# Kernel tuning notes

Hardware: AMD Instinct MI355X
Metric: run time of the kernel (lower is better)

The kernel has to match this reference:

```python
import jax, jax.numpy as jnp
import numpy as np

EPS = 1e-6  # rms_norm_eps
Q_EPS = 1e-5


def activation_quant(x):
    # per-token (last dim) absmax int8 quant
    scale = 127.0 / jnp.clip(jnp.max(jnp.abs(x), axis=-1, keepdims=True), Q_EPS, None)
    return jnp.clip(jnp.round(x * scale), -128, 127) / scale


def weight_quant(w):
    # ternary quant with global mean-absmax scale
    scale = 1.0 / jnp.clip(jnp.mean(jnp.abs(w)), Q_EPS, None)
    return jnp.clip(jnp.round(w * scale), -1, 1) / scale


def bit_linear(x, w):
    # straight-through estimator on both activation and weight quantization
    xq = x + jax.lax.stop_gradient(activation_quant(x) - x)
    wq = w + jax.lax.stop_gradient(weight_quant(w) - w)
    return jnp.einsum('...k,nk->...n', xq, wq)


def rmsnorm(x, w):
    var = jnp.mean(jnp.square(x), axis=-1, keepdims=True)
    return x * jax.lax.rsqrt(var + EPS) * w


def setup_inputs() -> dict:
    key = jax.random.key(0)
    ks = jax.random.split(key, 6)
    B, C, H, D, F, NC = 8, 3, 128, 2048, 8192, 1000
    return {
        'x': jax.random.normal(ks[0], (B, C, H, D), jnp.float32),
        'Wg': jax.random.normal(ks[1], (F, D), jnp.float32) * (D ** -0.5),
        'Wu': jax.random.normal(ks[2], (F, D), jnp.float32) * (D ** -0.5),
        'Wd': jax.random.normal(ks[3], (D, F), jnp.float32) * (F ** -0.5),
        'ln_w': jnp.ones((F,), jnp.float32),
        'cls_W': jax.random.normal(ks[4], (NC, C), jnp.float32) * (C ** -0.5),
        'cls_b': jnp.zeros((NC,), jnp.float32),
    }


def reference(x, Wg, Wu, Wd, ln_w, cls_W, cls_b):
    # BitNet SwiGLU MLP
    h = jax.nn.silu(bit_linear(x, Wg)) * bit_linear(x, Wu)  # [B,3,H,F]
    h = rmsnorm(h, ln_w)
    h = bit_linear(h, Wd)  # [B,3,H,D]
    # classifier: AdaptiveAvgPool2d((1,1)) over last two dims -> [B,3] -> Linear
    pooled = jnp.mean(h, axis=(2, 3))  # [B,3]
    return pooled @ cls_W.T + cls_b  # [B, num_classes]
```

## Files before the change

### kernel.cpp

```cpp
#include <hip/hip_runtime.h>
#include <stdint.h>

#define BB 8
#define CC 3
#define HH 128
#define DD 2048
#define FF 8192
#define NCLS 1000
#define MTOK (BB*CC*HH)
#define NW   (FF*DD)
#define INV_NW (1.0f/16777216.0f)

typedef __attribute__((ext_vector_type(4))) int i32x4;
typedef _Float16 f16x8 __attribute__((ext_vector_type(8)));

#define WS_SUMS    0
#define WS_POOLED  1024
#define WS_TSUM    16384
#define WS_INVSA   49152
#define WS_XQ      61440
#define WS_WGQ     6352896
#define WS_WUQ     23130112
#define WS_H       39907328
#define WS_NEED    90238976
#define WS_ZERO_BYTES 49152

__global__ __launch_bounds__(256) void abssum3_kernel(const float* __restrict__ Wg,
                                                      const float* __restrict__ Wu,
                                                      const float* __restrict__ Wd,
                                                      float* __restrict__ sums) {
  const float* w = (blockIdx.y == 0) ? Wg : (blockIdx.y == 1) ? Wu : Wd;
  const float4* w4 = (const float4*)w;
  const unsigned idx = blockIdx.x * 256 + threadIdx.x;
  float s0 = 0.f, s1 = 0.f, s2 = 0.f, s3 = 0.f;
#pragma unroll 4
  for (int it = 0; it < 64; it += 4) {
    float4 a = w4[idx + (size_t)(it + 0) * 65536];
    float4 b = w4[idx + (size_t)(it + 1) * 65536];
    float4 c = w4[idx + (size_t)(it + 2) * 65536];
    float4 d = w4[idx + (size_t)(it + 3) * 65536];
    s0 += fabsf(a.x) + fabsf(a.y) + fabsf(a.z) + fabsf(a.w);
    s1 += fabsf(b.x) + fabsf(b.y) + fabsf(b.z) + fabsf(b.w);
    s2 += fabsf(c.x) + fabsf(c.y) + fabsf(c.z) + fabsf(c.w);
    s3 += fabsf(d.x) + fabsf(d.y) + fabsf(d.z) + fabsf(d.w);
  }
  float s = (s0 + s1) + (s2 + s3);
  for (int off = 32; off > 0; off >>= 1) s += __shfl_xor(s, off);
  __shared__ float wsum[4];
  int wave = threadIdx.x >> 6, lane = threadIdx.x & 63;
  if (lane == 0) wsum[wave] = s;
  __syncthreads();
  if (threadIdx.x == 0)
    atomicAdd(&sums[blockIdx.y * 64], (wsum[0] + wsum[1]) + (wsum[2] + wsum[3]));
}

__global__ __launch_bounds__(256) void quant_x_kernel(const float* __restrict__ x,
                                                      int8_t* __restrict__ xq,
                                                      float* __restrict__ inv_sa) {
  const int tok = blockIdx.x, t = threadIdx.x;
  const float* row = x + (size_t)tok * DD;
  float4 v0 = *(const float4*)(row + t * 4);
  float4 v1 = *(const float4*)(row + 1024 + t * 4);
  float mx = fmaxf(fmaxf(fmaxf(fabsf(v0.x), fabsf(v0.y)), fmaxf(fabsf(v0.z), fabsf(v0.w))),
                   fmaxf(fmaxf(fabsf(v1.x), fabsf(v1.y)), fmaxf(fabsf(v1.z), fabsf(v1.w))));
  for (int off = 32; off > 0; off >>= 1) mx = fmaxf(mx, __shfl_xor(mx, off));
  __shared__ float wm[4];
  int wave = t >> 6, lane = t & 63;
  if (lane == 0) wm[wave] = mx;
  __syncthreads();
  float m = fmaxf(fmaxf(wm[0], wm[1]), fmaxf(wm[2], wm[3]));
  float mclip = fmaxf(m, 1e-5f);
  float sa = 127.0f / mclip;
  if (t == 0) inv_sa[tok] = mclip * (1.0f / 127.0f);
  float qv[8] = {v0.x, v0.y, v0.z, v0.w, v1.x, v1.y, v1.z, v1.w};
  unsigned p0 = 0, p1 = 0;
#pragma unroll
  for (int j = 0; j < 4; ++j) {
    int qi = (int)fminf(fmaxf(rintf(qv[j] * sa), -128.f), 127.f);
    p0 |= ((unsigned)(qi & 0xff)) << (8 * j);
  }
#pragma unroll
  for (int j = 0; j < 4; ++j) {
    int qi = (int)fminf(fmaxf(rintf(qv[4 + j] * sa), -128.f), 127.f);
    p1 |= ((unsigned)(qi & 0xff)) << (8 * j);
  }
  *(unsigned*)(xq + (size_t)tok * DD + t * 4) = p0;
  *(unsigned*)(xq + (size_t)tok * DD + 1024 + t * 4) = p1;
}

__global__ __launch_bounds__(256) void quant_gu_kernel(const float* __restrict__ Wg,
                                                       const float* __restrict__ Wu,
                                                       int8_t* __restrict__ wgq,
                                                       int8_t* __restrict__ wuq,
                                                       const float* __restrict__ sums) {
  const int mat = blockIdx.y;
  const float* w = mat ? Wu : Wg;
  int8_t* wq = mat ? wuq : wgq;
  const float scale = 1.0f / fmaxf(sums[mat * 64] * INV_NW, 1e-5f);
  const unsigned base = blockIdx.x * 4096;
  float4 v[4];
#pragma unroll
  for (int j = 0; j < 4; ++j)
    v[j] = *(const float4*)(w + base + j * 1024 + threadIdx.x * 4);
#pragma unroll
  for (int j = 0; j < 4; ++j) {
    float vv[4] = {v[j].x, v[j].y, v[j].z, v[j].w};
    unsigned p = 0;
#pragma unroll
    for (int jj = 0; jj < 4; ++jj) {
      int qi = (int)fminf(fmaxf(rintf(vv[jj] * scale), -1.f), 1.f);
      p |= ((unsigned)(qi & 0xff)) << (8 * jj);
    }
    *(unsigned*)(wq + base + j * 1024 + threadIdx.x * 4) = p;
  }
}

__global__ __launch_bounds__(256) void wd_colsum_kernel(const float* __restrict__ wd,
                                                        const float* __restrict__ sums,
                                                        float* __restrict__ tsum) {
  const float scale = 1.0f / fmaxf(sums[128] * INV_NW, 1e-5f);
  const int k = blockIdx.x * 256 + threadIdx.x;
  float acc = 0.f;
  const int d0 = blockIdx.y * 128;
  for (int d = d0; d < d0 + 128; ++d) {
    float w = wd[(size_t)d * FF + k];
    acc += fminf(fmaxf(rintf(w * scale), -1.f), 1.f);
  }
  atomicAdd(&tsum[k], acc);
}

__device__ __forceinline__ void gl_lds16(const void* g, void* l) {
  __builtin_amdgcn_global_load_lds((const __attribute__((address_space(1))) void*)g,
                                   (__attribute__((address_space(3))) void*)l, 16, 0, 0);
}

__global__ __launch_bounds__(256, 3) void gemm_gu_kernel(
    const int8_t* __restrict__ Aq,
    const int8_t* __restrict__ Bgq,
    const int8_t* __restrict__ Buq,
    const float* __restrict__ inv_sa,
    const float* __restrict__ sums,
    _Float16* __restrict__ Hbuf)
{
  __shared__ int8_t ldsA[128 * 128];
  __shared__ int8_t ldsG[64 * 128];
  __shared__ int8_t ldsU[64 * 128];

  const int t = threadIdx.x;
  const int wave = t >> 6, lane = t & 63;
  const int q = lane >> 4, ln = lane & 15;
  const int m0 = blockIdx.x * 128;
  const int n0 = blockIdx.y * 64;
  const int wm = (wave >> 1) * 64, wn = (wave & 1) * 32;

  i32x4 accg[4][2], accu[4][2];
#pragma unroll
  for (int i = 0; i < 4; ++i)
#pragma unroll
    for (int j = 0; j < 2; ++j) { accg[i][j] = i32x4{0,0,0,0}; accu[i][j] = i32x4{0,0,0,0}; }

  const int srow = lane >> 3;
  const int sp = lane & 7;

  for (int k0 = 0; k0 < DD; k0 += 128) {
    __syncthreads();
#pragma unroll
    for (int j = 0; j < 4; ++j) {
      const int rl = wave * 32 + j * 8 + srow;
      const int cg = sp ^ (rl & 7);
      gl_lds16(Aq + (size_t)(m0 + rl) * DD + k0 + cg * 16,
               ldsA + (wave * 32 + j * 8) * 128);
    }
#pragma unroll
    for (int j = 0; j < 2; ++j) {
      const int rl = wave * 16 + j * 8 + srow;
      const int cg = sp ^ (rl & 7);
      gl_lds16(Bgq + (size_t)(n0 + rl) * DD + k0 + cg * 16,
               ldsG + (wave * 16 + j * 8) * 128);
      gl_lds16(Buq + (size_t)(n0 + rl) * DD + k0 + cg * 16,
               ldsU + (wave * 16 + j * 8) * 128);
    }
    __syncthreads();

#pragma unroll
    for (int s = 0; s < 2; ++s) {
      i32x4 af[4], gf[2], uf[2];
#pragma unroll
      for (int mt = 0; mt < 4; ++mt) {
        const int row = wm + mt * 16 + ln;
        const int p = (s * 4 + q) ^ (row & 7);
        af[mt] = *(const i32x4*)(ldsA + row * 128 + p * 16);
      }
#pragma unroll
      for (int nt = 0; nt < 2; ++nt) {
        const int row = wn + nt * 16 + ln;
        const int p = (s * 4 + q) ^ (row & 7);
        gf[nt] = *(const i32x4*)(ldsG + row * 128 + p * 16);
        uf[nt] = *(const i32x4*)(ldsU + row * 128 + p * 16);
      }
#pragma unroll
      for (int mt = 0; mt < 4; ++mt)
#pragma unroll
        for (int nt = 0; nt < 2; ++nt) {
          accg[mt][nt] = __builtin_amdgcn_mfma_i32_16x16x64_i8(af[mt], gf[nt], accg[mt][nt], 0, 0, 0);
          accu[mt][nt] = __builtin_amdgcn_mfma_i32_16x16x64_i8(af[mt], uf[nt], accu[mt][nt], 0, 0, 0);
        }
    }
  }

  const float meanWg = fmaxf(sums[0] * INV_NW, 1e-5f);
  const float meanWu = fmaxf(sums[64] * INV_NW, 1e-5f);
#pragma unroll
  for (int mt = 0; mt < 4; ++mt) {
#pragma unroll
    for (int r = 0; r < 4; ++r) {
      const int row = m0 + wm + mt * 16 + q * 4 + r;
      const float isa = inv_sa[row];
      const float sg = isa * meanWg, su = isa * meanWu;
      _Float16* hrow = Hbuf + (size_t)row * FF + n0 + wn;
#pragma unroll
      for (int nt = 0; nt < 2; ++nt) {
        const float g = (float)accg[mt][nt][r] * sg;
        const float u = (float)accu[mt][nt][r] * su;
        const float sv = g / (1.0f + expf(-g));
        hrow[nt * 16 + ln] = (_Float16)(sv * u);
      }
    }
  }
}

__global__ __launch_bounds__(256) void rms_quant_dot_kernel(
    const _Float16* __restrict__ H, const float* __restrict__ lnw,
    const float* __restrict__ tsum, float* __restrict__ pooled) {
  const int tok = blockIdx.x, t = threadIdx.x;
  const _Float16* row = H + (size_t)tok * FF;
  f16x8 hv[4];
  float4 lw[8];
  float ssq = 0.f, mx = 0.f;
#pragma unroll
  for (int i = 0; i < 4; ++i) {
    hv[i] = *(const f16x8*)(row + i * 2048 + t * 8);
    lw[2 * i] = *(const float4*)(lnw + i * 2048 + t * 8);
    lw[2 * i + 1] = *(const float4*)(lnw + i * 2048 + t * 8 + 4);
#pragma unroll
    for (int j = 0; j < 8; ++j) {
      float h = (float)hv[i][j];
      float w = (j < 4) ? ((const float*)&lw[2 * i])[j] : ((const float*)&lw[2 * i + 1])[j - 4];
      ssq += h * h;
      mx = fmaxf(mx, fabsf(h * w));
    }
  }
  for (int off = 32; off > 0; off >>= 1) {
    ssq += __shfl_xor(ssq, off);
    mx = fmaxf(mx, __shfl_xor(mx, off));
  }
  __shared__ float rs[4], rm[4], ra[4];
  const int wave = t >> 6, lane = t & 63;
  if (lane == 0) { rs[wave] = ssq; rm[wave] = mx; }
  __syncthreads();
  const float S = (rs[0] + rs[1]) + (rs[2] + rs[3]);
  const float M = fmaxf(fmaxf(rm[0], rm[1]), fmaxf(rm[2], rm[3]));
  const float r = rsqrtf(S * (1.0f / (float)FF) + 1e-6f);
  const float mc = fmaxf(M * r, 1e-5f);
  const float as2 = 127.0f / mc;
  float acc = 0.f;
#pragma unroll
  for (int i = 0; i < 4; ++i) {
    float4 t0 = *(const float4*)(tsum + i * 2048 + t * 8);
    float4 t1 = *(const float4*)(tsum + i * 2048 + t * 8 + 4);
    const float* tw = (const float*)&t0;
    const float* lwp = (const float*)&lw[2 * i];
#pragma unroll
    for (int j = 0; j < 8; ++j) {
      float ts = (j < 4) ? tw[j] : ((const float*)&t1)[j - 4];
      float w = lwp[j];
      float y = (float)hv[i][j] * w * r;
      acc += fminf(fmaxf(rintf(y * as2), -128.f), 127.f) * ts;
    }
  }
  for (int off = 32; off > 0; off >>= 1) acc += __shfl_xor(acc, off);
  if (lane == 0) ra[wave] = acc;
  __syncthreads();
  if (t == 0)
    pooled[tok] = ((ra[0] + ra[1]) + (ra[2] + ra[3])) * (mc * (1.0f / 127.0f));
}

__global__ __launch_bounds__(256) void classifier_kernel(
    const float* __restrict__ pooled, const float* __restrict__ sums,
    const float* __restrict__ clsW, const float* __restrict__ clsb,
    float* __restrict__ out) {
  const int b = blockIdx.x, t = threadIdx.x;
  const float meanWd = fmaxf(sums[128] * INV_NW, 1e-5f);
  const float sc = meanWd * (1.0f / (float)(HH * DD));
  __shared__ float ps[3];
#pragma unroll
  for (int c = 0; c < 3; ++c) {
    float s = 0.f;
    if (t < 64) {
      const float* base = pooled + (b * 3 + c) * 128;
      s = base[t] + base[t + 64];
    }
    if (t < 64) {
      for (int off = 32; off > 0; off >>= 1) s += __shfl_xor(s, off);
      if (t == 0) ps[c] = s * sc;
    }
    __syncthreads();
  }
  const float p0 = ps[0], p1 = ps[1], p2 = ps[2];
  for (int n = t; n < NCLS; n += 256)
    out[b * NCLS + n] = clsb[n] + p0 * clsW[n * 3 + 0] + p1 * clsW[n * 3 + 1] + p2 * clsW[n * 3 + 2];
}

extern "C" void kernel_launch(void* const* d_in, const int* in_sizes, int n_in,
                              void* d_out, int out_size, void* d_ws, size_t ws_size,
                              hipStream_t stream) {
  if (n_in < 7 || ws_size < (size_t)WS_NEED) return;
  const float* x = (const float*)d_in[0];
  const float* Wg = (const float*)d_in[1];
  const float* Wu = (const float*)d_in[2];
  const float* Wd = (const float*)d_in[3];
  const float* lnw = (const float*)d_in[4];
  const float* clsW = (const float*)d_in[5];
  const float* clsb = (const float*)d_in[6];
  float* out = (float*)d_out;
  char* ws = (char*)d_ws;
  float* sums = (float*)(ws + WS_SUMS);
  float* pooled = (float*)(ws + WS_POOLED);
  float* tsum = (float*)(ws + WS_TSUM);
  float* inv_sa = (float*)(ws + WS_INVSA);
  int8_t* xq = (int8_t*)(ws + WS_XQ);
  int8_t* wgq = (int8_t*)(ws + WS_WGQ);
  int8_t* wuq = (int8_t*)(ws + WS_WUQ);
  _Float16* hbuf = (_Float16*)(ws + WS_H);

  hipMemsetAsync(ws, 0, WS_ZERO_BYTES, stream);
  abssum3_kernel<<<dim3(256, 3), 256, 0, stream>>>(Wg, Wu, Wd, sums);
  quant_x_kernel<<<MTOK, 256, 0, stream>>>(x, xq, inv_sa);
  quant_gu_kernel<<<dim3(4096, 2), 256, 0, stream>>>(Wg, Wu, wgq, wuq, sums);
  wd_colsum_kernel<<<dim3(32, 16), 256, 0, stream>>>(Wd, sums, tsum);
  gemm_gu_kernel<<<dim3(24, 128), 256, 0, stream>>>(xq, wgq, wuq, inv_sa, sums, hbuf);
  rms_quant_dot_kernel<<<MTOK, 256, 0, stream>>>(hbuf, lnw, tsum, pooled);
  classifier_kernel<<<BB, 256, 0, stream>>>(pooled, sums, clsW, clsb, out);
  (void)in_sizes; (void)out_size;
}
```

Baseline: 387.2 us.

## Fuse prep kernels, drop memset/atomics, switch GEMM to 32x32 int8 MFMA

Merges the abs-sum, x quantization and tsum zeroing into one prep kernel that writes per-block partial sums instead of using atomics. Weight quantization and the Wd column-sum share a second kernel, with each block re-reducing the partials to get its scale. The gate/up GEMM switches from 16x16x64 to 32x32x32 int8 MFMA and raises launch bounds occupancy to 4. This cuts launches and the memset, and changes the GEMM inner-loop shape, but each block now repeats a partial-sum reduction and the higher occupancy target may squeeze registers.

```diff
diff --git a/kernel.cpp b/kernel.cpp
--- a/kernel.cpp
+++ b/kernel.cpp
@@ -12,10 +12,12 @@
 #define INV_NW (1.0f/16777216.0f)
 
 typedef __attribute__((ext_vector_type(4))) int i32x4;
+typedef __attribute__((ext_vector_type(16))) int i32x16;
 typedef _Float16 f16x8 __attribute__((ext_vector_type(8)));
 
 #define WS_SUMS    0
-#define WS_POOLED  1024
+#define WS_PART    256
+#define WS_POOLED  4096
 #define WS_TSUM    16384
 #define WS_INVSA   49152
 #define WS_XQ      61440
@@ -23,110 +25,125 @@
 #define WS_WUQ     23130112
 #define WS_H       39907328
 #define WS_NEED    90238976
-#define WS_ZERO_BYTES 49152
-
-__global__ __launch_bounds__(256) void abssum3_kernel(const float* __restrict__ Wg,
-                                                      const float* __restrict__ Wu,
-                                                      const float* __restrict__ Wd,
-                                                      float* __restrict__ sums) {
-  const float* w = (blockIdx.y == 0) ? Wg : (blockIdx.y == 1) ? Wu : Wd;
-  const float4* w4 = (const float4*)w;
-  const unsigned idx = blockIdx.x * 256 + threadIdx.x;
-  float s0 = 0.f, s1 = 0.f, s2 = 0.f, s3 = 0.f;
+
+__device__ __forceinline__ float reduce256(float v, float* red, bool first) {
+  for (int off = 32; off > 0; off >>= 1) v += __shfl_xor(v, off);
+  if (!first) __syncthreads();
+  if ((threadIdx.x & 63) == 0) red[threadIdx.x >> 6] = v;
+  __syncthreads();
+  return (red[0] + red[1]) + (red[2] + red[3]);
+}
+
+__global__ __launch_bounds__(256) void prep_kernel(
+    const float* __restrict__ Wg, const float* __restrict__ Wu,
+    const float* __restrict__ Wd, const float* __restrict__ x,
+    float* __restrict__ part, int8_t* __restrict__ xq,
+    float* __restrict__ inv_sa, float* __restrict__ tsum) {
+  const int bx = blockIdx.x, t = threadIdx.x;
+  if (bx < 768) {
+    const int mat = bx >> 8;
+    const float* w = (mat == 0) ? Wg : (mat == 1) ? Wu : Wd;
+    const float4* w4 = (const float4*)w;
+    const unsigned idx = (bx & 255) * 256 + t;
+    float s0 = 0.f, s1 = 0.f, s2 = 0.f, s3 = 0.f;
 #pragma unroll 4
-  for (int it = 0; it < 64; it += 4) {
-    float4 a = w4[idx + (size_t)(it + 0) * 65536];
-    float4 b = w4[idx + (size_t)(it + 1) * 65536];
-    float4 c = w4[idx + (size_t)(it + 2) * 65536];
-    float4 d = w4[idx + (size_t)(it + 3) * 65536];
-    s0 += fabsf(a.x) + fabsf(a.y) + fabsf(a.z) + fabsf(a.w);
-    s1 += fabsf(b.x) + fabsf(b.y) + fabsf(b.z) + fabsf(b.w);
-    s2 += fabsf(c.x) + fabsf(c.y) + fabsf(c.z) + fabsf(c.w);
-    s3 += fabsf(d.x) + fabsf(d.y) + fabsf(d.z) + fabsf(d.w);
-  }
-  float s = (s0 + s1) + (s2 + s3);
-  for (int off = 32; off > 0; off >>= 1) s += __shfl_xor(s, off);
-  __shared__ float wsum[4];
-  int wave = threadIdx.x >> 6, lane = threadIdx.x & 63;
-  if (lane == 0) wsum[wave] = s;
-  __syncthreads();
-  if (threadIdx.x == 0)
-    atomicAdd(&sums[blockIdx.y * 64], (wsum[0] + wsum[1]) + (wsum[2] + wsum[3]));
-}
-
-__global__ __launch_bounds__(256) void quant_x_kernel(const float* __restrict__ x,
-                                                      int8_t* __restrict__ xq,
-                                                      float* __restrict__ inv_sa) {
-  const int tok = blockIdx.x, t = threadIdx.x;
-  const float* row = x + (size_t)tok * DD;
-  float4 v0 = *(const float4*)(row + t * 4);
-  float4 v1 = *(const float4*)(row + 1024 + t * 4);
-  float mx = fmaxf(fmaxf(fmaxf(fabsf(v0.x), fabsf(v0.y)), fmaxf(fabsf(v0.z), fabsf(v0.w))),
-                   fmaxf(fmaxf(fabsf(v1.x), fabsf(v1.y)), fmaxf(fabsf(v1.z), fabsf(v1.w))));
-  for (int off = 32; off > 0; off >>= 1) mx = fmaxf(mx, __shfl_xor(mx, off));
-  __shared__ float wm[4];
-  int wave = t >> 6, lane = t & 63;
-  if (lane == 0) wm[wave] = mx;
-  __syncthreads();
-  float m = fmaxf(fmaxf(wm[0], wm[1]), fmaxf(wm[2], wm[3]));
-  float mclip = fmaxf(m, 1e-5f);
-  float sa = 127.0f / mclip;
-  if (t == 0) inv_sa[tok] = mclip * (1.0f / 127.0f);
-  float qv[8] = {v0.x, v0.y, v0.z, v0.w, v1.x, v1.y, v1.z, v1.w};
-  unsigned p0 = 0, p1 = 0;
-#pragma unroll
-  for (int j = 0; j < 4; ++j) {
-    int qi = (int)fminf(fmaxf(rintf(qv[j] * sa), -128.f), 127.f);
-    p0 |= ((unsigned)(qi & 0xff)) << (8 * j);
-  }
-#pragma unroll
-  for (int j = 0; j < 4; ++j) {
-    int qi = (int)fminf(fmaxf(rintf(qv[4 + j] * sa), -128.f), 127.f);
-    p1 |= ((unsigned)(qi & 0xff)) << (8 * j);
-  }
-  *(unsigned*)(xq + (size_t)tok * DD + t * 4) = p0;
-  *(unsigned*)(xq + (size_t)tok * DD + 1024 + t * 4) = p1;
-}
-
-__global__ __launch_bounds__(256) void quant_gu_kernel(const float* __restrict__ Wg,
-                                                       const float* __restrict__ Wu,
-                                                       int8_t* __restrict__ wgq,
-                                                       int8_t* __restrict__ wuq,
-                                                       const float* __restrict__ sums) {
-  const int mat = blockIdx.y;
-  const float* w = mat ? Wu : Wg;
-  int8_t* wq = mat ? wuq : wgq;
-  const float scale = 1.0f / fmaxf(sums[mat * 64] * INV_NW, 1e-5f);
-  const unsigned base = blockIdx.x * 4096;
-  float4 v[4];
-#pragma unroll
-  for (int j = 0; j < 4; ++j)
-    v[j] = *(const float4*)(w + base + j * 1024 + threadIdx.x * 4);
-#pragma unroll
-  for (int j = 0; j < 4; ++j) {
-    float vv[4] = {v[j].x, v[j].y, v[j].z, v[j].w};
-    unsigned p = 0;
-#pragma unroll
-    for (int jj = 0; jj < 4; ++jj) {
-      int qi = (int)fminf(fmaxf(rintf(vv[jj] * scale), -1.f), 1.f);
-      p |= ((unsigned)(qi & 0xff)) << (8 * jj);
-    }
-    *(unsigned*)(wq + base + j * 1024 + threadIdx.x * 4) = p;
-  }
-}
-
-__global__ __launch_bounds__(256) void wd_colsum_kernel(const float* __restrict__ wd,
-                                                        const float* __restrict__ sums,
-                                                        float* __restrict__ tsum) {
-  const float scale = 1.0f / fmaxf(sums[128] * INV_NW, 1e-5f);
-  const int k = blockIdx.x * 256 + threadIdx.x;
-  float acc = 0.f;
-  const int d0 = blockIdx.y * 128;
-  for (int d = d0; d < d0 + 128; ++d) {
-    float w = wd[(size_t)d * FF + k];
-    acc += fminf(fmaxf(rintf(w * scale), -1.f), 1.f);
-  }
-  atomicAdd(&tsum[k], acc);
+    for (int it = 0; it < 64; it += 4) {
+      float4 a = w4[idx + (size_t)(it + 0) * 65536];
+      float4 b = w4[idx + (size_t)(it + 1) * 65536];
+      float4 c = w4[idx + (size_t)(it + 2) * 65536];
+      float4 d = w4[idx + (size_t)(it + 3) * 65536];
+      s0 += fabsf(a.x) + fabsf(a.y) + fabsf(a.z) + fabsf(a.w);
+      s1 += fabsf(b.x) + fabsf(b.y) + fabsf(b.z) + fabsf(b.w);
+      s2 += fabsf(c.x) + fabsf(c.y) + fabsf(c.z) + fabsf(c.w);
+      s3 += fabsf(d.x) + fabsf(d.y) + fabsf(d.z) + fabsf(d.w);
+    }
+    __shared__ float red[4];
+    float total = reduce256((s0 + s1) + (s2 + s3), red, true);
+    if (t == 0) part[bx] = total;
+  } else if (bx < 3840) {
+    const int tok = bx - 768;
+    const float* row = x + (size_t)tok * DD;
+    float4 v0 = *(const float4*)(row + t * 4);
+    float4 v1 = *(const float4*)(row + 1024 + t * 4);
+    float mx = fmaxf(fmaxf(fmaxf(fabsf(v0.x), fabsf(v0.y)), fmaxf(fabsf(v0.z), fabsf(v0.w))),
+                     fmaxf(fmaxf(fabsf(v1.x), fabsf(v1.y)), fmaxf(fabsf(v1.z), fabsf(v1.w))));
+    for (int off = 32; off > 0; off >>= 1) mx = fmaxf(mx, __shfl_xor(mx, off));
+    __shared__ float wm[4];
+    if ((t & 63) == 0) wm[t >> 6] = mx;
+    __syncthreads();
+    float m = fmaxf(fmaxf(wm[0], wm[1]), fmaxf(wm[2], wm[3]));
+    float mclip = fmaxf(m, 1e-5f);
+    float sa = 127.0f / mclip;
+    if (t == 0) inv_sa[tok] = mclip * (1.0f / 127.0f);
+    float qv[8] = {v0.x, v0.y, v0.z, v0.w, v1.x, v1.y, v1.z, v1.w};
+    unsigned p0 = 0, p1 = 0;
+#pragma unroll
+    for (int j = 0; j < 4; ++j) {
+      int qi = (int)fminf(fmaxf(rintf(qv[j] * sa), -128.f), 127.f);
+      p0 |= ((unsigned)(qi & 0xff)) << (8 * j);
+    }
+#pragma unroll
+    for (int j = 0; j < 4; ++j) {
+      int qi = (int)fminf(fmaxf(rintf(qv[4 + j] * sa), -128.f), 127.f);
+      p1 |= ((unsigned)(qi & 0xff)) << (8 * j);
+    }
+    *(unsigned*)(xq + (size_t)tok * DD + t * 4) = p0;
+    *(unsigned*)(xq + (size_t)tok * DD + 1024 + t * 4) = p1;
+  } else {
+    float4 z = {0.f, 0.f, 0.f, 0.f};
+#pragma unroll
+    for (int j = 0; j < 8; ++j)
+      *(float4*)(tsum + j * 1024 + t * 4) = z;
+  }
+}
+
+__global__ __launch_bounds__(256) void wquant_kernel(
+    const float* __restrict__ Wg, const float* __restrict__ Wu,
+    const float* __restrict__ Wd, const float* __restrict__ part,
+    float* __restrict__ sums, int8_t* __restrict__ wgq,
+    int8_t* __restrict__ wuq, float* __restrict__ tsum) {
+  const int bx = blockIdx.x, t = threadIdx.x;
+  __shared__ float red[4];
+  if (bx < 8192) {
+    const int mat = bx >> 12;
+    const float* w = mat ? Wu : Wg;
+    int8_t* wq = mat ? wuq : wgq;
+    const float total = reduce256(part[mat * 256 + t], red, true);
+    const float scale = 1.0f / fmaxf(total * INV_NW, 1e-5f);
+    const unsigned base = (bx & 4095) * 4096;
+    float4 v[4];
+#pragma unroll
+    for (int j = 0; j < 4; ++j)
+      v[j] = *(const float4*)(w + base + j * 1024 + t * 4);
+#pragma unroll
+    for (int j = 0; j < 4; ++j) {
+      float vv[4] = {v[j].x, v[j].y, v[j].z, v[j].w};
+      unsigned p = 0;
+#pragma unroll
+      for (int jj = 0; jj < 4; ++jj) {
+        int qi = (int)fminf(fmaxf(rintf(vv[jj] * scale), -1.f), 1.f);
+        p |= ((unsigned)(qi & 0xff)) << (8 * jj);
+      }
+      *(unsigned*)(wq + base + j * 1024 + t * 4) = p;
+    }
+  } else {
+    const int idx = bx - 8192;
+    const int slab = idx >> 5, colg = idx & 31;
+    const float totalWd = reduce256(part[512 + t], red, true);
+    const float scale = 1.0f / fmaxf(totalWd * INV_NW, 1e-5f);
+    const int col = colg * 256 + t;
+    const float* wp = Wd + (size_t)(slab * 256) * FF + col;
+    float acc = 0.f;
+#pragma unroll 8
+    for (int d = 0; d < 256; ++d)
+      acc += fminf(fmaxf(rintf(wp[(size_t)d * FF] * scale), -1.f), 1.f);
+    atomicAdd(&tsum[col], acc);
+    if (idx == 255) {
+      const float tg = reduce256(part[t], red, false);
+      const float tu = reduce256(part[256 + t], red, false);
+      if (t == 0) { sums[0] = tg; sums[1] = tu; sums[2] = totalWd; }
+    }
+  }
 }
 
 __device__ __forceinline__ void gl_lds16(const void* g, void* l) {
@@ -134,7 +151,7 @@
                                    (__attribute__((address_space(3))) void*)l, 16, 0, 0);
 }
 
-__global__ __launch_bounds__(256, 3) void gemm_gu_kernel(
+__global__ __launch_bounds__(256, 4) void gemm_gu_kernel(
     const int8_t* __restrict__ Aq,
     const int8_t* __restrict__ Bgq,
     const int8_t* __restrict__ Buq,
@@ -148,16 +165,16 @@
 
   const int t = threadIdx.x;
   const int wave = t >> 6, lane = t & 63;
-  const int q = lane >> 4, ln = lane & 15;
+  const int l32 = lane & 31, l5 = lane >> 5;
   const int m0 = blockIdx.x * 128;
   const int n0 = blockIdx.y * 64;
   const int wm = (wave >> 1) * 64, wn = (wave & 1) * 32;
 
-  i32x4 accg[4][2], accu[4][2];
-#pragma unroll
-  for (int i = 0; i < 4; ++i)
-#pragma unroll
-    for (int j = 0; j < 2; ++j) { accg[i][j] = i32x4{0,0,0,0}; accu[i][j] = i32x4{0,0,0,0}; }
+  i32x16 accg[2], accu[2];
+#pragma unroll
+  for (int i = 0; i < 2; ++i)
+#pragma unroll
+    for (int r = 0; r < 16; ++r) { accg[i][r] = 0; accu[i][r] = 0; }
 
   const int srow = lane >> 3;
   const int sp = lane & 7;
@@ -183,48 +200,41 @@
     __syncthreads();
 
 #pragma unroll
-    for (int s = 0; s < 2; ++s) {
-      i32x4 af[4], gf[2], uf[2];
-#pragma unroll
-      for (int mt = 0; mt < 4; ++mt) {
-        const int row = wm + mt * 16 + ln;
-        const int p = (s * 4 + q) ^ (row & 7);
+    for (int ks = 0; ks < 4; ++ks) {
+      i32x4 af[2], gfv, ufv;
+#pragma unroll
+      for (int mt = 0; mt < 2; ++mt) {
+        const int row = wm + mt * 32 + l32;
+        const int p = (ks * 2 + l5) ^ (row & 7);
         af[mt] = *(const i32x4*)(ldsA + row * 128 + p * 16);
       }
-#pragma unroll
-      for (int nt = 0; nt < 2; ++nt) {
-        const int row = wn + nt * 16 + ln;
-        const int p = (s * 4 + q) ^ (row & 7);
-        gf[nt] = *(const i32x4*)(ldsG + row * 128 + p * 16);
-        uf[nt] = *(const i32x4*)(ldsU + row * 128 + p * 16);
+      {
+        const int row = wn + l32;
+        const int p = (ks * 2 + l5) ^ (row & 7);
+        gfv = *(const i32x4*)(ldsG + row * 128 + p * 16);
+        ufv = *(const i32x4*)(ldsU + row * 128 + p * 16);
       }
 #pragma unroll
-      for (int mt = 0; mt < 4; ++mt)
-#pragma unroll
-        for (int nt = 0; nt < 2; ++nt) {
-          accg[mt][nt] = __builtin_amdgcn_mfma_i32_16x16x64_i8(af[mt], gf[nt], accg[mt][nt], 0, 0, 0);
-          accu[mt][nt] = __builtin_amdgcn_mfma_i32_16x16x64_i8(af[mt], uf[nt], accu[mt][nt], 0, 0, 0);
-        }
+      for (int mt = 0; mt < 2; ++mt) {
+        accg[mt] = __builtin_amdgcn_mfma_i32_32x32x32_i8(af[mt], gfv, accg[mt], 0, 0, 0);
+        accu[mt] = __builtin_amdgcn_mfma_i32_32x32x32_i8(af[mt], ufv, accu[mt], 0, 0, 0);
+      }
     }
   }
 
   const float meanWg = fmaxf(sums[0] * INV_NW, 1e-5f);
-  const float meanWu = fmaxf(sums[64] * INV_NW, 1e-5f);
-#pragma unroll
-  for (int mt = 0; mt < 4; ++mt) {
-#pragma unroll
-    for (int r = 0; r < 4; ++r) {
-      const int row = m0 + wm + mt * 16 + q * 4 + r;
+  const float meanWu = fmaxf(sums[1] * INV_NW, 1e-5f);
+  const int coln = n0 + wn + l32;
+#pragma unroll
+  for (int mt = 0; mt < 2; ++mt) {
+#pragma unroll
+    for (int r = 0; r < 16; ++r) {
+      const int row = m0 + wm + mt * 32 + (r & 3) + 8 * (r >> 2) + 4 * l5;
       const float isa = inv_sa[row];
-      const float sg = isa * meanWg, su = isa * meanWu;
-      _Float16* hrow = Hbuf + (size_t)row * FF + n0 + wn;
-#pragma unroll
-      for (int nt = 0; nt < 2; ++nt) {
-        const float g = (float)accg[mt][nt][r] * sg;
-        const float u = (float)accu[mt][nt][r] * su;
-        const float sv = g / (1.0f + expf(-g));
-        hrow[nt * 16 + ln] = (_Float16)(sv * u);
-      }
+      const float g = (float)accg[mt][r] * (isa * meanWg);
+      const float u = (float)accu[mt][r] * (isa * meanWu);
+      const float sv = g / (1.0f + expf(-g));
+      Hbuf[(size_t)row * FF + coln] = (_Float16)(sv * u);
     }
   }
 }
@@ -242,12 +252,12 @@
     hv[i] = *(const f16x8*)(row + i * 2048 + t * 8);
     lw[2 * i] = *(const float4*)(lnw + i * 2048 + t * 8);
     lw[2 * i + 1] = *(const float4*)(lnw + i * 2048 + t * 8 + 4);
+    const float* lwp = (const float*)&lw[2 * i];
 #pragma unroll
     for (int j = 0; j < 8; ++j) {
       float h = (float)hv[i][j];
-      float w = (j < 4) ? ((const float*)&lw[2 * i])[j] : ((const float*)&lw[2 * i + 1])[j - 4];
       ssq += h * h;
-      mx = fmaxf(mx, fabsf(h * w));
+      mx = fmaxf(mx, fabsf(h * lwp[j]));
     }
   }
   for (int off = 32; off > 0; off >>= 1) {
@@ -268,13 +278,13 @@
   for (int i = 0; i < 4; ++i) {
     float4 t0 = *(const float4*)(tsum + i * 2048 + t * 8);
     float4 t1 = *(const float4*)(tsum + i * 2048 + t * 8 + 4);
-    const float* tw = (const float*)&t0;
     const float* lwp = (const float*)&lw[2 * i];
+    const float* tp0 = (const float*)&t0;
+    const float* tp1 = (const float*)&t1;
 #pragma unroll
     for (int j = 0; j < 8; ++j) {
-      float ts = (j < 4) ? tw[j] : ((const float*)&t1)[j - 4];
-      float w = lwp[j];
-      float y = (float)hv[i][j] * w * r;
+      float ts = (j < 4) ? tp0[j] : tp1[j - 4];
+      float y = (float)hv[i][j] * lwp[j] * r;
       acc += fminf(fmaxf(rintf(y * as2), -128.f), 127.f) * ts;
     }
   }
@@ -290,7 +300,7 @@
     const float* __restrict__ clsW, const float* __restrict__ clsb,
     float* __restrict__ out) {
   const int b = blockIdx.x, t = threadIdx.x;
-  const float meanWd = fmaxf(sums[128] * INV_NW, 1e-5f);
+  const float meanWd = fmaxf(sums[2] * INV_NW, 1e-5f);
   const float sc = meanWd * (1.0f / (float)(HH * DD));
   __shared__ float ps[3];
 #pragma unroll
@@ -299,8 +309,6 @@
     if (t < 64) {
       const float* base = pooled + (b * 3 + c) * 128;
       s = base[t] + base[t + 64];
-    }
-    if (t < 64) {
       for (int off = 32; off > 0; off >>= 1) s += __shfl_xor(s, off);
       if (t == 0) ps[c] = s * sc;
     }
@@ -325,6 +333,7 @@
   float* out = (float*)d_out;
   char* ws = (char*)d_ws;
   float* sums = (float*)(ws + WS_SUMS);
+  float* part = (float*)(ws + WS_PART);
   float* pooled = (float*)(ws + WS_POOLED);
   float* tsum = (float*)(ws + WS_TSUM);
   float* inv_sa = (float*)(ws + WS_INVSA);
@@ -333,11 +342,8 @@
   int8_t* wuq = (int8_t*)(ws + WS_WUQ);
   _Float16* hbuf = (_Float16*)(ws + WS_H);
 
-  hipMemsetAsync(ws, 0, WS_ZERO_BYTES, stream);
-  abssum3_kernel<<<dim3(256, 3), 256, 0, stream>>>(Wg, Wu, Wd, sums);
-  quant_x_kernel<<<MTOK, 256, 0, stream>>>(x, xq, inv_sa);
-  quant_gu_kernel<<<dim3(4096, 2), 256, 0, stream>>>(Wg, Wu, wgq, wuq, sums);
-  wd_colsum_kernel<<<dim3(32, 16), 256, 0, stream>>>(Wd, sums, tsum);
+  prep_kernel<<<3841, 256, 0, stream>>>(Wg, Wu, Wd, x, part, xq, inv_sa, tsum);
+  wquant_kernel<<<8448, 256, 0, stream>>>(Wg, Wu, Wd, part, sums, wgq, wuq, tsum);
   gemm_gu_kernel<<<dim3(24, 128), 256, 0, stream>>>(xq, wgq, wuq, inv_sa, sums, hbuf);
   rms_quant_dot_kernel<<<MTOK, 256, 0, stream>>>(hbuf, lnw, tsum, pooled);
   classifier_kernel<<<BB, 256, 0, stream>>>(pooled, sums, clsW, clsb, out);
```

Measured after the change: 392.4 us. Within noise of the previous version (+1.4%).
